# Optimization experiments

Hardware: AMD Instinct MI355X
Metric: run time of the kernel (lower is better)

Reference implementation:

```python
import jax, jax.numpy as jnp
import numpy as np

N = 4096
PED_SPEED = 1.34   # desired pedestrian speed (m/s)
K = 2.0            # goal-attraction gain
ALPHA = 10.66      # repulsion strength
PED_RADIUS = 0.3
PED_MASS = 60.0
BETTA = 0.71       # repulsion range
DT = 0.4
COST_A = 1.0       # goal-progress weight
COST_B = 1.0       # blame (proximity) weight
COST_E = 1.0       # blame length scale
EPS = 1e-8


def calc_forces(state, goals):
    pos = state[:, 0:2]            # [N,2]
    vel = state[:, 2:4]            # [N,2]
    # O(N^2) pairwise social repulsion
    delta = pos[:, None, :] - pos[None, :, :]                    # [N,N,2]
    dist = jnp.sqrt(jnp.sum(delta * delta, axis=-1) + EPS)       # [N,N]
    mag = ALPHA * jnp.exp((2.0 * PED_RADIUS - dist) / BETTA)     # [N,N]
    mag = mag * (1.0 - jnp.eye(pos.shape[0], dtype=pos.dtype))   # zero self-force
    rep_force = jnp.sum((mag / dist)[..., None] * delta, axis=1)  # [N,2]
    # attraction toward goal: relax velocity to desired velocity
    to_goal = goals - pos
    gd = jnp.sqrt(jnp.sum(to_goal * to_goal, axis=-1, keepdims=True) + EPS)
    attr_force = K * PED_MASS * (PED_SPEED * to_goal / gd - vel)
    return rep_force, attr_force


def pose_propagation(F, state):
    pos = state[:, 0:2]
    vel = state[:, 2:4]
    vel_new = vel + (F / PED_MASS) * DT
    speed = jnp.sqrt(jnp.sum(vel_new * vel_new, axis=-1, keepdims=True) + EPS)
    vel_new = vel_new * jnp.minimum(1.0, PED_SPEED / speed)  # clamp to max speed
    pos_new = pos + vel_new * DT
    return jnp.concatenate([pos_new, vel_new], axis=1)      # [N,4]


def calc_cost_function(goals, robot_init_pose, state, observed_state):
    pos = state[:, 0:2]
    robot_pose = pos[0]  # agent 0 is the robot
    goal_vec = goals[0] - robot_init_pose
    pg = jnp.dot(pos[0] - robot_init_pose, goal_vec) / (jnp.sqrt(jnp.sum(goal_vec * goal_vec)) + EPS)
    dist_rp = jnp.sqrt(jnp.sum((pos - robot_pose) ** 2, axis=-1) + EPS)  # [N]
    blame = COST_B * jnp.exp(-dist_rp / COST_E)
    dev = jnp.sum((pos - observed_state[:, 0:2]) ** 2, axis=-1)
    return -COST_A * pg + blame + dev  # [N]


def setup_inputs():
    key = jax.random.key(0)
    k1, k2, k3, k4 = jax.random.split(key, 4)
    scale = jnp.array([10.0, 10.0, 1.0, 1.0], dtype=jnp.float32)
    state = jax.random.normal(k1, (N, 4), dtype=jnp.float32) * scale
    goals = jax.random.normal(k2, (N, 2), dtype=jnp.float32) * 10.0
    robot_init_pose = jax.random.normal(k3, (2,), dtype=jnp.float32) * 10.0
    observed_state = jax.random.normal(k4, (N, 4), dtype=jnp.float32) * scale
    cost = jnp.zeros((N, 1), dtype=jnp.float32)
    return {"state": state, "cost": cost, "goals": goals,
            "robot_init_pose": robot_init_pose, "observed_state": observed_state}


def reference(state, cost, goals, robot_init_pose, observed_state):
    rf, af = calc_forces(state, goals)
    F = rf + af
    out = pose_propagation(F, state)
    temp = calc_cost_function(goals, robot_init_pose, out, observed_state)
    cost_new = cost + temp.reshape(-1, 1)
    return out, cost_new
```

## Files before the change

### kernel.cpp

```cpp
#include <hip/hip_runtime.h>

#define N 4096
#define NBJ 64
#define EPS 1e-8f

__global__ __launch_bounds__(256) void rep_pairs(const float4* __restrict__ state4,
                                                 float2* __restrict__ part) {
    __shared__ float2 sj[64];
    const int tid = threadIdx.x;
    const int jb  = blockIdx.y;
    const int i   = blockIdx.x * 256 + tid;

    if (tid < 64) {
        const float4 s = state4[jb * 64 + tid];
        sj[tid] = make_float2(s.x, s.y);
    }
    const float4 si = state4[i];
    const float xi = si.x, yi = si.y;
    __syncthreads();

    const float C1 = 1.44269504088896340736f / 0.71f;
    const float C0 = 0.6f * C1 + 3.41414351f;

    float fx0 = 0.f, fy0 = 0.f, fx1 = 0.f, fy1 = 0.f;
#pragma unroll 8
    for (int jj = 0; jj < 64; jj += 2) {
        {
            const float2 pj = sj[jj];
            const float dx   = xi - pj.x;
            const float dy   = yi - pj.y;
            const float r2   = fmaf(dx, dx, fmaf(dy, dy, EPS));
            const float inv  = __builtin_amdgcn_rsqf(r2);
            const float d    = r2 * inv;
            const float coef = __builtin_amdgcn_exp2f(fmaf(d, -C1, C0)) * inv;
            fx0 = fmaf(coef, dx, fx0);
            fy0 = fmaf(coef, dy, fy0);
        }
        {
            const float2 pj = sj[jj + 1];
            const float dx   = xi - pj.x;
            const float dy   = yi - pj.y;
            const float r2   = fmaf(dx, dx, fmaf(dy, dy, EPS));
            const float inv  = __builtin_amdgcn_rsqf(r2);
            const float d    = r2 * inv;
            const float coef = __builtin_amdgcn_exp2f(fmaf(d, -C1, C0)) * inv;
            fx1 = fmaf(coef, dx, fx1);
            fy1 = fmaf(coef, dy, fy1);
        }
    }
    part[(size_t)jb * N + i] = make_float2(fx0 + fx1, fy0 + fy1);
}

__global__ __launch_bounds__(256) void finalize(const float* __restrict__ state,
                                                const float* __restrict__ cost_in,
                                                const float* __restrict__ goals,
                                                const float* __restrict__ rip,
                                                const float4* __restrict__ obs4,
                                                const float2* __restrict__ part,
                                                float* __restrict__ out) {
    __shared__ float2 red[2][128];
    __shared__ float2 s_p0;
    const int tid = threadIdx.x;
    const int il  = tid & 127;
    const int ks  = tid >> 7;
    const int i   = blockIdx.x * 128 + il;

    float fx = 0.f, fy = 0.f;
    for (int k = ks * 32; k < ks * 32 + 32; ++k) {
        const float2 p = part[(size_t)k * N + i];
        fx += p.x; fy += p.y;
    }
    red[ks][il] = make_float2(fx, fy);

    if (tid < 64) {
        float2 f0 = part[(size_t)tid * N + 0];
#pragma unroll
        for (int off = 32; off > 0; off >>= 1) {
            f0.x += __shfl_down(f0.x, off);
            f0.y += __shfl_down(f0.y, off);
        }
        if (tid == 0) {
            const float px = state[0], py = state[1], vx = state[2], vy = state[3];
            const float gx = goals[0] - px, gy = goals[1] - py;
            const float gd = sqrtf(fmaf(gx, gx, fmaf(gy, gy, EPS)));
            const float Fx = f0.x + 120.f * (1.34f * gx / gd - vx);
            const float Fy = f0.y + 120.f * (1.34f * gy / gd - vy);
            float vnx = fmaf(Fx, 0.4f / 60.f, vx);
            float vny = fmaf(Fy, 0.4f / 60.f, vy);
            const float sp  = sqrtf(fmaf(vnx, vnx, fmaf(vny, vny, EPS)));
            const float fac = fminf(1.f, 1.34f / sp);
            vnx *= fac; vny *= fac;
            s_p0 = make_float2(fmaf(vnx, 0.4f, px), fmaf(vny, 0.4f, py));
        }
    }
    __syncthreads();

    if (ks == 0) {
        fx += red[1][il].x;
        fy += red[1][il].y;

        const float px = state[i * 4 + 0], py = state[i * 4 + 1];
        const float vx = state[i * 4 + 2], vy = state[i * 4 + 3];
        const float gx = goals[i * 2 + 0] - px, gy = goals[i * 2 + 1] - py;
        const float gd = sqrtf(fmaf(gx, gx, fmaf(gy, gy, EPS)));
        fx += 120.f * (1.34f * gx / gd - vx);
        fy += 120.f * (1.34f * gy / gd - vy);
        float vnx = fmaf(fx, 0.4f / 60.f, vx);
        float vny = fmaf(fy, 0.4f / 60.f, vy);
        const float sp  = sqrtf(fmaf(vnx, vnx, fmaf(vny, vny, EPS)));
        const float fac = fminf(1.f, 1.34f / sp);
        vnx *= fac; vny *= fac;
        const float pnx = fmaf(vnx, 0.4f, px);
        const float pny = fmaf(vny, 0.4f, py);

        out[i * 4 + 0] = pnx;
        out[i * 4 + 1] = pny;
        out[i * 4 + 2] = vnx;
        out[i * 4 + 3] = vny;

        const float rx = rip[0], ry = rip[1];
        const float gvx = goals[0] - rx, gvy = goals[1] - ry;
        const float p0x = s_p0.x, p0y = s_p0.y;
        const float pg = ((p0x - rx) * gvx + (p0y - ry) * gvy)
                       / (sqrtf(gvx * gvx + gvy * gvy) + EPS);
        const float ddx = pnx - p0x, ddy = pny - p0y;
        const float dist_rp = sqrtf(fmaf(ddx, ddx, fmaf(ddy, ddy, EPS)));
        const float blame = __expf(-dist_rp);
        const float4 ob = obs4[i];
        const float dev = (pnx - ob.x) * (pnx - ob.x) + (pny - ob.y) * (pny - ob.y);

        out[4 * N + i] = cost_in[i] + (-pg + blame + dev);
    }
}

extern "C" void kernel_launch(void* const* d_in, const int* in_sizes, int n_in,
                              void* d_out, int out_size, void* d_ws, size_t ws_size,
                              hipStream_t stream) {
    const float* state = (const float*)d_in[0];
    const float* cost  = (const float*)d_in[1];
    const float* goals = (const float*)d_in[2];
    const float* rip   = (const float*)d_in[3];
    const float* obs   = (const float*)d_in[4];
    float* out   = (float*)d_out;
    float2* part = (float2*)d_ws;

    rep_pairs<<<dim3(16, NBJ), 256, 0, stream>>>((const float4*)state, part);
    finalize<<<N / 128, 256, 0, stream>>>(state, cost, goals, rip,
                                          (const float4*)state == nullptr ? nullptr : (const float4*)d_in[4],
                                          part, out);
}
```

Baseline: 70.33 us.

## Fuse pairwise and finalize kernels via last-block atomic counter reduction

Merges the pairwise repulsion kernel and the finalize kernel into one launch. Each j-block bumps a per-row-block atomic counter, and the last block to arrive reduces the 64 partial sums and runs the integration and cost computation. This removes the second kernel launch and the dependency gap between the two launches. In exchange it adds a memset launch, threadfences, a serial 64-step reduction done by a single block per row group, and a grid-wide ordering dependency.

New measurement: 134.9 us. 91.7% more time.

```diff
diff --git a/kernel.cpp b/kernel.cpp
--- a/kernel.cpp
+++ b/kernel.cpp
@@ -4,12 +4,26 @@
 #define NBJ 64
 #define EPS 1e-8f
 
-__global__ __launch_bounds__(256) void rep_pairs(const float4* __restrict__ state4,
-                                                 float2* __restrict__ part) {
+typedef unsigned long long u64;
+
+__global__ __launch_bounds__(256) void social_force(
+    const float4* __restrict__ state4,
+    const float*  __restrict__ cost_in,
+    const float*  __restrict__ goals,
+    const float*  __restrict__ rip,
+    const float4* __restrict__ obs4,
+    int*          __restrict__ cnt,
+    float2*       __restrict__ part,
+    float*        __restrict__ out)
+{
     __shared__ float2 sj[64];
+    __shared__ int    s_last;
+    __shared__ float2 s_p0;
+
     const int tid = threadIdx.x;
+    const int ib  = blockIdx.x;
     const int jb  = blockIdx.y;
-    const int i   = blockIdx.x * 256 + tid;
+    const int i   = ib * 256 + tid;
 
     if (tid < 64) {
         const float4 s = state4[jb * 64 + tid];
@@ -49,88 +63,79 @@
         }
     }
     part[(size_t)jb * N + i] = make_float2(fx0 + fx1, fy0 + fy1);
-}
 
-__global__ __launch_bounds__(256) void finalize(const float* __restrict__ state,
-                                                const float* __restrict__ cost_in,
-                                                const float* __restrict__ goals,
-                                                const float* __restrict__ rip,
-                                                const float4* __restrict__ obs4,
-                                                const float2* __restrict__ part,
-                                                float* __restrict__ out) {
-    __shared__ float2 red[2][128];
-    __shared__ float2 s_p0;
-    const int tid = threadIdx.x;
-    const int il  = tid & 127;
-    const int ks  = tid >> 7;
-    const int i   = blockIdx.x * 128 + il;
+    __threadfence();
+    if (tid == 0)
+        s_last = (atomicAdd(&cnt[ib], 1) == NBJ - 1) ? 1 : 0;
+    __syncthreads();
+    if (!s_last) return;
+    __threadfence();
 
-    float fx = 0.f, fy = 0.f;
-    for (int k = ks * 32; k < ks * 32 + 32; ++k) {
-        const float2 p = part[(size_t)k * N + i];
-        fx += p.x; fy += p.y;
+    const u64* pp = (const u64*)part;
+
+    float Fx = 0.f, Fy = 0.f;
+    for (int k = 0; k < NBJ; ++k) {
+        const u64 raw = __hip_atomic_load(pp + (size_t)k * N + i,
+                                          __ATOMIC_RELAXED, __HIP_MEMORY_SCOPE_AGENT);
+        const float2 p = __builtin_bit_cast(float2, raw);
+        Fx += p.x; Fy += p.y;
     }
-    red[ks][il] = make_float2(fx, fy);
 
     if (tid < 64) {
-        float2 f0 = part[(size_t)tid * N + 0];
+        const u64 raw = __hip_atomic_load(pp + (size_t)tid * N,
+                                          __ATOMIC_RELAXED, __HIP_MEMORY_SCOPE_AGENT);
+        float2 f0 = __builtin_bit_cast(float2, raw);
 #pragma unroll
         for (int off = 32; off > 0; off >>= 1) {
             f0.x += __shfl_down(f0.x, off);
             f0.y += __shfl_down(f0.y, off);
         }
         if (tid == 0) {
-            const float px = state[0], py = state[1], vx = state[2], vy = state[3];
-            const float gx = goals[0] - px, gy = goals[1] - py;
+            const float4 s0 = state4[0];
+            const float gx = goals[0] - s0.x, gy = goals[1] - s0.y;
             const float gd = sqrtf(fmaf(gx, gx, fmaf(gy, gy, EPS)));
-            const float Fx = f0.x + 120.f * (1.34f * gx / gd - vx);
-            const float Fy = f0.y + 120.f * (1.34f * gy / gd - vy);
-            float vnx = fmaf(Fx, 0.4f / 60.f, vx);
-            float vny = fmaf(Fy, 0.4f / 60.f, vy);
+            const float Fx0 = f0.x + 120.f * (1.34f * gx / gd - s0.z);
+            const float Fy0 = f0.y + 120.f * (1.34f * gy / gd - s0.w);
+            float vnx = fmaf(Fx0, 0.4f / 60.f, s0.z);
+            float vny = fmaf(Fy0, 0.4f / 60.f, s0.w);
             const float sp  = sqrtf(fmaf(vnx, vnx, fmaf(vny, vny, EPS)));
             const float fac = fminf(1.f, 1.34f / sp);
             vnx *= fac; vny *= fac;
-            s_p0 = make_float2(fmaf(vnx, 0.4f, px), fmaf(vny, 0.4f, py));
+            s_p0 = make_float2(fmaf(vnx, 0.4f, s0.x), fmaf(vny, 0.4f, s0.y));
         }
     }
     __syncthreads();
 
-    if (ks == 0) {
-        fx += red[1][il].x;
-        fy += red[1][il].y;
+    const float px = si.x, py = si.y, vx = si.z, vy = si.w;
+    const float gx = goals[i * 2 + 0] - px, gy = goals[i * 2 + 1] - py;
+    const float gd = sqrtf(fmaf(gx, gx, fmaf(gy, gy, EPS)));
+    Fx += 120.f * (1.34f * gx / gd - vx);
+    Fy += 120.f * (1.34f * gy / gd - vy);
+    float vnx = fmaf(Fx, 0.4f / 60.f, vx);
+    float vny = fmaf(Fy, 0.4f / 60.f, vy);
+    const float sp  = sqrtf(fmaf(vnx, vnx, fmaf(vny, vny, EPS)));
+    const float fac = fminf(1.f, 1.34f / sp);
+    vnx *= fac; vny *= fac;
+    const float pnx = fmaf(vnx, 0.4f, px);
+    const float pny = fmaf(vny, 0.4f, py);
 
-        const float px = state[i * 4 + 0], py = state[i * 4 + 1];
-        const float vx = state[i * 4 + 2], vy = state[i * 4 + 3];
-        const float gx = goals[i * 2 + 0] - px, gy = goals[i * 2 + 1] - py;
-        const float gd = sqrtf(fmaf(gx, gx, fmaf(gy, gy, EPS)));
-        fx += 120.f * (1.34f * gx / gd - vx);
-        fy += 120.f * (1.34f * gy / gd - vy);
-        float vnx = fmaf(fx, 0.4f / 60.f, vx);
-        float vny = fmaf(fy, 0.4f / 60.f, vy);
-        const float sp  = sqrtf(fmaf(vnx, vnx, fmaf(vny, vny, EPS)));
-        const float fac = fminf(1.f, 1.34f / sp);
-        vnx *= fac; vny *= fac;
-        const float pnx = fmaf(vnx, 0.4f, px);
-        const float pny = fmaf(vny, 0.4f, py);
+    out[i * 4 + 0] = pnx;
+    out[i * 4 + 1] = pny;
+    out[i * 4 + 2] = vnx;
+    out[i * 4 + 3] = vny;
 
-        out[i * 4 + 0] = pnx;
-        out[i * 4 + 1] = pny;
-        out[i * 4 + 2] = vnx;
-        out[i * 4 + 3] = vny;
+    const float rx = rip[0], ry = rip[1];
+    const float gvx = goals[0] - rx, gvy = goals[1] - ry;
+    const float p0x = s_p0.x, p0y = s_p0.y;
+    const float pg = ((p0x - rx) * gvx + (p0y - ry) * gvy)
+                   / (sqrtf(gvx * gvx + gvy * gvy) + EPS);
+    const float ddx = pnx - p0x, ddy = pny - p0y;
+    const float dist_rp = sqrtf(fmaf(ddx, ddx, fmaf(ddy, ddy, EPS)));
+    const float blame = __expf(-dist_rp);
+    const float4 ob = obs4[i];
+    const float dev = (pnx - ob.x) * (pnx - ob.x) + (pny - ob.y) * (pny - ob.y);
 
-        const float rx = rip[0], ry = rip[1];
-        const float gvx = goals[0] - rx, gvy = goals[1] - ry;
-        const float p0x = s_p0.x, p0y = s_p0.y;
-        const float pg = ((p0x - rx) * gvx + (p0y - ry) * gvy)
-                       / (sqrtf(gvx * gvx + gvy * gvy) + EPS);
-        const float ddx = pnx - p0x, ddy = pny - p0y;
-        const float dist_rp = sqrtf(fmaf(ddx, ddx, fmaf(ddy, ddy, EPS)));
-        const float blame = __expf(-dist_rp);
-        const float4 ob = obs4[i];
-        const float dev = (pnx - ob.x) * (pnx - ob.x) + (pny - ob.y) * (pny - ob.y);
-
-        out[4 * N + i] = cost_in[i] + (-pg + blame + dev);
-    }
+    out[4 * N + i] = cost_in[i] + (-pg + blame + dev);
 }
 
 extern "C" void kernel_launch(void* const* d_in, const int* in_sizes, int n_in,
@@ -142,10 +147,12 @@
     const float* rip   = (const float*)d_in[3];
     const float* obs   = (const float*)d_in[4];
     float* out   = (float*)d_out;
-    float2* part = (float2*)d_ws;
 
-    rep_pairs<<<dim3(16, NBJ), 256, 0, stream>>>((const float4*)state, part);
-    finalize<<<N / 128, 256, 0, stream>>>(state, cost, goals, rip,
-                                          (const float4*)state == nullptr ? nullptr : (const float4*)d_in[4],
-                                          part, out);
+    int*    cnt  = (int*)d_ws;
+    float2* part = (float2*)((char*)d_ws + 256);
+
+    hipMemsetAsync(d_ws, 0, 256, stream);
+    social_force<<<dim3(16, NBJ), 256, 0, stream>>>(
+        (const float4*)state, cost, goals, rip, (const float4*)obs,
+        cnt, part, out);
 }
```
